# Kernel tuning notes

Hardware: AMD Instinct MI355X
Metric: run time of the kernel (lower is better)

The kernel has to match this reference:

```python
import jax, jax.numpy as jnp
import numpy as np

B, L, D_IN, H, N_BLOCKS, N_STATE, PRED = 2048, 168, 9, 96, 4, 96, 96
N2 = N_STATE // 2  # complex-conjugate pairs: keep half the state, double the real part


def s4d_kernel(log_dt, log_A_real, A_imag, C_re, C_im, length):
    # S4D (diagonal SSM) convolution kernel, ZOH-style discretization.
    dt = jnp.exp(log_dt)[:, None]                  # (H,1)
    A = -jnp.exp(log_A_real) + 1j * A_imag         # (H,N2)
    C = C_re + 1j * C_im                           # (H,N2)
    dtA = dt * A                                   # (H,N2)
    Ct = C * (jnp.exp(dtA) - 1.0) / A              # discretized C
    # Vandermonde: K[h,l] = 2*Re(sum_n Ct[h,n] * exp(dtA[h,n] * l))
    V = jnp.exp(dtA[:, :, None] * jnp.arange(length))  # (H,N2,L)
    return 2.0 * jnp.einsum('hn,hnl->hl', Ct, V).real  # (H,L)


def causal_conv(u, K):
    # u: (B,L,H), K: (H,L) -> causal depthwise convolution via FFT
    n = 2 * u.shape[1]
    Uf = jnp.fft.rfft(u, n=n, axis=1)              # (B,n/2+1,H)
    Kf = jnp.fft.rfft(K.T, n=n, axis=0)            # (n/2+1,H)
    return jnp.fft.irfft(Uf * Kf[None], n=n, axis=1)[:, :u.shape[1]]


def layer_norm(x, w, b):
    mu = x.mean(-1, keepdims=True)
    var = x.var(-1, keepdims=True)
    return (x - mu) / jnp.sqrt(var + 1e-5) * w + b


def setup_inputs() -> dict:
    key = jax.random.key(0)
    ks = jax.random.split(key, 20)
    r = lambda k, s, sc=1.0: jax.random.normal(k, s, jnp.float32) * sc
    inp = {
        'x': r(ks[0], (B, L, D_IN)),
        'enc_W': r(ks[1], (D_IN, H), 1.0 / np.sqrt(D_IN)),
        'enc_b': jnp.zeros((H,), jnp.float32),
        # per-block S4D parameters, stacked on leading n_blocks axis
        'log_dt': jax.random.uniform(ks[2], (N_BLOCKS, H), jnp.float32,
                                     np.log(1e-3), np.log(1e-1)),
        'log_A_real': jnp.full((N_BLOCKS, H, N2), np.log(0.5), jnp.float32),
        'A_imag': jnp.tile(np.pi * jnp.arange(N2, dtype=jnp.float32), (N_BLOCKS, H, 1)),
        'C_re': r(ks[3], (N_BLOCKS, H, N2), 0.5),
        'C_im': r(ks[4], (N_BLOCKS, H, N2), 0.5),
        'D_skip': r(ks[5], (N_BLOCKS, H)),
        'W_out': r(ks[6], (N_BLOCKS, H, H), 1.0 / np.sqrt(H)),
        'b_out': jnp.zeros((N_BLOCKS, H), jnp.float32),
        'ln_w': jnp.ones((N_BLOCKS, H), jnp.float32),
        'ln_b': jnp.zeros((N_BLOCKS, H), jnp.float32),
        'dec_W': r(ks[7], (H, H), 1.0 / np.sqrt(H)),
        'dec_b': jnp.zeros((H,), jnp.float32),
        'fc1_W': r(ks[8], (H * L, H), 1.0 / np.sqrt(H * L)),
        'fc1_b': jnp.zeros((H,), jnp.float32),
        'fc2_W': r(ks[9], (H, PRED), 1.0 / np.sqrt(H)),
        'fc2_b': jnp.zeros((PRED,), jnp.float32),
    }
    return inp


def reference(x, enc_W, enc_b, log_dt, log_A_real, A_imag, C_re, C_im, D_skip,
              W_out, b_out, ln_w, ln_b, dec_W, dec_b, fc1_W, fc1_b, fc2_W, fc2_b):
    h = x @ enc_W + enc_b                              # (B,L,H) encoder
    for i in range(N_BLOCKS):                          # post-norm residual S4 blocks
        K = s4d_kernel(log_dt[i], log_A_real[i], A_imag[i], C_re[i], C_im[i], L)
        z = causal_conv(h, K) + h * D_skip[i]          # SSM conv + skip D*u
        z = jax.nn.gelu(z)                             # activation (dropout off at eval)
        z = z @ W_out[i] + b_out[i]                    # output mixing
        h = layer_norm(h + z, ln_w[i], ln_b[i])        # residual + post-norm
    h = h @ dec_W + dec_b                              # S4Model decoder (d_model->d_model)
    out = h.reshape(h.shape[0], -1) @ fc1_W + fc1_b    # flatten + fc1
    out = out @ fc2_W + fc2_b                          # fc2 -> PRED_LEN
    return out[..., None]                              # (B,96,1)
```

## Files before the change

kernel.cpp:

```cpp
#include <hip/hip_runtime.h>
#include <hip/hip_bf16.h>
#include <math.h>

#define NB 4
#define B  2048
#define L  168
#define DI 9
#define H  96
#define N2 48

#define ZSTR2 132

typedef short short8 __attribute__((ext_vector_type(8)));
typedef float f32x4  __attribute__((ext_vector_type(4)));
typedef unsigned short u16x8 __attribute__((ext_vector_type(8)));
typedef unsigned short u16x4 __attribute__((ext_vector_type(4)));

__device__ __forceinline__ float gelu_f(float x) {
    float x3 = x * x * x;
    float y  = 0.7978845608028654f * (x + 0.044715f * x3);
    float ey = __expf(2.0f * y);
    float t  = 1.0f - 2.0f / (ey + 1.0f);
    return 0.5f * x * (1.0f + t);
}

__device__ __forceinline__ unsigned short bf16_rne(float x) {
    unsigned u = __float_as_uint(x);
    return (unsigned short)((u + 0x7FFFu + ((u >> 16) & 1u)) >> 16);
}
__device__ __forceinline__ float b2f(unsigned short v) {
    return __uint_as_float((unsigned)v << 16);
}

__global__ void kgen_kernel(const float* __restrict__ log_dt, const float* __restrict__ lar,
                            const float* __restrict__ aim, const float* __restrict__ cre,
                            const float* __restrict__ cim, float* __restrict__ K)
{
    const int ih   = blockIdx.x;
    const int lane = threadIdx.x;
    float ctre = 0.f, ctim = 0.f, pre = 0.f, pim = 0.f, mre = 0.f, mim = 0.f;
    if (lane < N2) {
        float dt  = expf(log_dt[ih]);
        int   idx = ih * N2 + lane;
        float reA = -expf(lar[idx]);
        float imA = aim[idx];
        float dre = dt * reA, dim = dt * imA;
        float er  = expf(dre);
        float sv, cv;
        sincosf(dim, &sv, &cv);
        mre = er * cv; mim = er * sv;
        float nre = mre - 1.0f, nim = mim;
        float den = reA * reA + imA * imA;
        float tre = (nre * reA + nim * imA) / den;
        float tim = (nim * reA - nre * imA) / den;
        float cr = cre[idx], ci = cim[idx];
        ctre = cr * tre - ci * tim;
        ctim = cr * tim + ci * tre;
        pre = 1.0f; pim = 0.0f;
    }
    float* Kr = K + ih * L;
    for (int l = 0; l < L; ++l) {
        float term = ctre * pre - ctim * pim;
        #pragma unroll
        for (int off = 32; off > 0; off >>= 1) term += __shfl_xor(term, off, 64);
        if (lane == 0) Kr[l] = 2.0f * term;
        float nr = pre * mre - pim * mim;
        float ni = pre * mim + pim * mre;
        pre = nr; pim = ni;
    }
}

__global__ void wprep_kernel(const float* __restrict__ wout, short* __restrict__ wfrag, int ntask)
{
    int idx = blockIdx.x * 256 + threadIdx.x;
    if (idx >= ntask) return;
    int layer = idx / 9216;  int rem  = idx - layer * 9216;
    int ch    = rem / 3072;  int rem2 = rem - ch * 3072;
    int m     = rem2 / 512;  int rem3 = rem2 - m * 512;
    int s     = rem3 / 256;  int rem4 = rem3 - s * 256;
    int lane  = rem4 / 4;    int d    = rem4 - lane * 4;
    int g = lane >> 4, c = lane & 15;
    int k  = ch * 32 + g * 8 + 2 * d;
    int hp = m * 16 + c;
    const float* Wl = wout + (size_t)layer * H * H;
    float w0 = Wl[k * H + hp];
    float w1 = Wl[(k + 1) * H + hp];
    unsigned short b0, b1;
    if (s == 0) { b0 = bf16_rne(w0); b1 = bf16_rne(w1); }
    else {
        unsigned short h0 = bf16_rne(w0), h1 = bf16_rne(w1);
        b0 = bf16_rne(w0 - b2f(h0));
        b1 = bf16_rne(w1 - b2f(h1));
    }
    wfrag[idx * 2]     = (short)b0;
    wfrag[idx * 2 + 1] = (short)b1;
}

__global__ void tgen_kernel(const float* __restrict__ Kg, short* __restrict__ tfrag)
{
    static const int kmaxA[11] = {0, 0, 1, 1, 2, 2, 3, 3, 4, 4, 5};
    static const int toffA[11] = {0, 1, 2, 4, 6, 9, 12, 16, 20, 25, 30};
    int idx = blockIdx.x * 256 + threadIdx.x;
    if (idx >= 96 * 66 * 64) return;
    int lane = idx & 63;
    int t    = (idx >> 6) % 66;
    int h    = (idx >> 6) / 66;
    int mi = t / 6, ki = t - mi * 6;
    if (ki > kmaxA[mi]) return;
    int g = lane >> 4, c = lane & 15;
    int row = mi * 16 + c;
    short8 a;
    #pragma unroll
    for (int j = 0; j < 8; ++j) {
        int kk = ki * 32 + g * 8 + j;
        int d  = row - kk;
        float val = (row < L && d >= 0) ? Kg[h * L + d] : 0.0f;
        a[j] = (short)bf16_rne(val);
    }
    short8* dst = (short8*)tfrag + (size_t)(h * 36 + toffA[mi] + ki) * 64;
    dst[lane] = a;
}

__launch_bounds__(256)
__global__ void wcomp_kernel(const float* __restrict__ decW, const float* __restrict__ decb,
                             const float* __restrict__ fc1W, float* __restrict__ wcs,
                             float* __restrict__ cbpart)
{
    __shared__ float Bs[96 * 100];
    const int tid = threadIdx.x;
    const int l   = blockIdx.x;
    for (int e = tid; e < 96 * 96; e += 256) {
        int h = e / 96, p = e - h * 96;
        Bs[h * 100 + p] = fc1W[(size_t)(l * 96 + h) * 96 + p];
    }
    __syncthreads();
    const int pt = tid & 31;
    const int kt = tid >> 5;
    float acc[12][3];
    #pragma unroll
    for (int kk = 0; kk < 12; ++kk)
        #pragma unroll
        for (int j = 0; j < 3; ++j) acc[kk][j] = 0.f;
    for (int h = 0; h < 96; ++h) {
        float dw[12];
        #pragma unroll
        for (int kk = 0; kk < 12; ++kk) dw[kk] = decW[(kt + 8 * kk) * 96 + h];
        float bs[3];
        #pragma unroll
        for (int j = 0; j < 3; ++j) bs[j] = Bs[h * 100 + pt + 32 * j];
        #pragma unroll
        for (int kk = 0; kk < 12; ++kk)
            #pragma unroll
            for (int j = 0; j < 3; ++j) acc[kk][j] = fmaf(dw[kk], bs[j], acc[kk][j]);
    }
    float* wl = wcs + (size_t)l * 9216;
    #pragma unroll
    for (int kk = 0; kk < 12; ++kk)
        #pragma unroll
        for (int j = 0; j < 3; ++j)
            wl[(kt + 8 * kk) * 96 + pt + 32 * j] = acc[kk][j];
    if (kt == 0) {
        #pragma unroll
        for (int j = 0; j < 3; ++j) {
            float s = 0.f;
            for (int h = 0; h < 96; ++h) s = fmaf(decb[h], Bs[h * 100 + pt + 32 * j], s);
            cbpart[l * 96 + pt + 32 * j] = s;
        }
    }
}

__global__ void cbias_red_kernel(const float* __restrict__ cbpart, const float* __restrict__ fc1b,
                                 float* __restrict__ cbias)
{
    int p = threadIdx.x;
    if (p < 96) {
        float s = fc1b[p];
        for (int l = 0; l < L; ++l) s += cbpart[l * 96 + p];
        cbias[p] = s;
    }
}

__launch_bounds__(256)
__global__ void enc2_kernel(const float* __restrict__ x, const float* __restrict__ W,
                            const float* __restrict__ bias, unsigned short* __restrict__ hb2)
{
    __shared__ float Ws[DI * H];
    __shared__ float bs[H];
    const int tid = threadIdx.x;
    const int l   = blockIdx.x;
    const int b0  = blockIdx.y * 256;
    for (int e = tid; e < DI * H; e += 256) Ws[e] = W[e];
    if (tid < H) bs[tid] = bias[tid];
    __syncthreads();
    float xv[DI];
    const float* xr = x + (size_t)(b0 + tid) * (L * DI) + l * DI;
    #pragma unroll
    for (int k = 0; k < DI; ++k) xv[k] = xr[k];
    for (int h = 0; h < H; ++h) {
        float a = bs[h];
        #pragma unroll
        for (int k = 0; k < DI; ++k) a = fmaf(xv[k], Ws[k * H + h], a);
        hb2[((size_t)h * L + l) * B + b0 + tid] = bf16_rne(a);
    }
}

__launch_bounds__(512)
__global__ void conv3_kernel(const unsigned short* __restrict__ hb2, const short* __restrict__ tfrag,
                             const float* __restrict__ Dsk, unsigned short* __restrict__ z2)
{
    static const int toffA[11] = {0, 1, 2, 4, 6, 9, 12, 16, 20, 25, 30};
    __shared__ __align__(16) unsigned short zs[192 * ZSTR2];
    const int tid  = threadIdx.x;
    const int w    = tid >> 6;
    const int lane = tid & 63;
    const int g    = lane >> 4;
    const int cc   = lane & 15;
    const int h    = blockIdx.x;
    const int b0   = blockIdx.y * 128;

    for (int e = tid; e < 168 * 16; e += 512) {
        int lp = e >> 4, b8 = e & 15;
        u16x8 v = *(const u16x8*)(hb2 + ((size_t)h * L + lp) * B + b0 + b8 * 8);
        *(u16x4*)(&zs[lp * ZSTR2 + b8 * 8])     = (u16x4){v[0], v[1], v[2], v[3]};
        *(u16x4*)(&zs[lp * ZSTR2 + b8 * 8 + 4]) = (u16x4){v[4], v[5], v[6], v[7]};
    }
    for (int e = tid; e < 24 * 16; e += 512) {
        int lp = 168 + (e >> 4), b8 = e & 15;
        *(u16x4*)(&zs[lp * ZSTR2 + b8 * 8])     = (u16x4){0, 0, 0, 0};
        *(u16x4*)(&zs[lp * ZSTR2 + b8 * 8 + 4]) = (u16x4){0, 0, 0, 0};
    }
    __syncthreads();

    f32x4 acc[11];
    #pragma unroll
    for (int mi = 0; mi < 11; ++mi) acc[mi] = (f32x4){0.f, 0.f, 0.f, 0.f};

    const int col = w * 16 + cc;

    #pragma unroll
    for (int ki = 0; ki < 6; ++ki) {
        short8 bh;
        #pragma unroll
        for (int j = 0; j < 8; ++j)
            bh[j] = (short)zs[(ki * 32 + g * 8 + j) * ZSTR2 + col];
        #pragma unroll
        for (int mi = 2 * ki; mi < 11; ++mi) {
            const short8* Tf = (const short8*)(tfrag) + (size_t)(h * 36 + toffA[mi] + ki) * 64;
            short8 ah = Tf[lane];
            acc[mi] = __builtin_amdgcn_mfma_f32_16x16x32_bf16(ah, bh, acc[mi], 0, 0, 0);
        }
    }

    const float ds = Dsk[h];
    #pragma unroll
    for (int mi = 0; mi < 11; ++mi) {
        #pragma unroll
        for (int r = 0; r < 4; ++r) {
            int l = mi * 16 + g * 4 + r;
            if (l < L) {
                float uu = b2f(zs[l * ZSTR2 + col]);
                float zv = gelu_f(fmaf(ds, uu, acc[mi][r]));
                zs[l * ZSTR2 + col] = bf16_rne(zv);
            }
        }
    }
    __syncthreads();
    for (int e = tid; e < 168 * 16; e += 512) {
        int lp = e >> 4, b8 = e & 15;
        u16x4 a = *(const u16x4*)(&zs[lp * ZSTR2 + b8 * 8]);
        u16x4 b = *(const u16x4*)(&zs[lp * ZSTR2 + b8 * 8 + 4]);
        u16x8 v = {a[0], a[1], a[2], a[3], b[0], b[1], b[2], b[3]};
        *(u16x8*)(z2 + ((size_t)h * L + lp) * B + b0 + b8 * 8) = v;
    }
}

__launch_bounds__(512)
__global__ void mix2_kernel(const unsigned short* __restrict__ z2, unsigned short* __restrict__ hb2,
                            const short* __restrict__ wfrag, const float* __restrict__ bout,
                            const float* __restrict__ lnw, const float* __restrict__ lnb)
{
    __shared__ __align__(16) unsigned short zs[H * ZSTR2];
    __shared__ __align__(16) unsigned short rs[H * ZSTR2];
    const int tid  = threadIdx.x;
    const int w    = tid >> 6;
    const int lane = tid & 63;
    const int g    = lane >> 4;
    const int cc   = lane & 15;
    const int l    = blockIdx.x;
    const int b0   = blockIdx.y * 128;

    for (int e = tid; e < 96 * 16; e += 512) {
        int hh = e >> 4, b8 = e & 15;
        u16x8 v = *(const u16x8*)(z2 + ((size_t)hh * L + l) * B + b0 + b8 * 8);
        *(u16x4*)(&zs[hh * ZSTR2 + b8 * 8])     = (u16x4){v[0], v[1], v[2], v[3]};
        *(u16x4*)(&zs[hh * ZSTR2 + b8 * 8 + 4]) = (u16x4){v[4], v[5], v[6], v[7]};
    }
    for (int e = tid; e < 96 * 16; e += 512) {
        int hh = e >> 4, b8 = e & 15;
        u16x8 v = *(const u16x8*)(hb2 + ((size_t)hh * L + l) * B + b0 + b8 * 8);
        *(u16x4*)(&rs[hh * ZSTR2 + b8 * 8])     = (u16x4){v[0], v[1], v[2], v[3]};
        *(u16x4*)(&rs[hh * ZSTR2 + b8 * 8 + 4]) = (u16x4){v[4], v[5], v[6], v[7]};
    }
    __syncthreads();

    f32x4 acc[6];
    #pragma unroll
    for (int m = 0; m < 6; ++m) acc[m] = (f32x4){0.f, 0.f, 0.f, 0.f};

    const int col = w * 16 + cc;

    #pragma unroll
    for (int ks = 0; ks < 3; ++ks) {
        short8 bh;
        #pragma unroll
        for (int j = 0; j < 8; ++j)
            bh[j] = (short)zs[(ks * 32 + g * 8 + j) * ZSTR2 + col];
        const short8* Wf = (const short8*)(wfrag) + ks * 12 * 64;
        #pragma unroll
        for (int m = 0; m < 6; ++m) {
            short8 ah = Wf[(m * 2 + 0) * 64 + lane];
            short8 al = Wf[(m * 2 + 1) * 64 + lane];
            acc[m] = __builtin_amdgcn_mfma_f32_16x16x32_bf16(al, bh, acc[m], 0, 0, 0);
            acc[m] = __builtin_amdgcn_mfma_f32_16x16x32_bf16(ah, bh, acc[m], 0, 0, 0);
        }
    }

    float vals[6][4];
    float s = 0.f, q = 0.f;
    #pragma unroll
    for (int m = 0; m < 6; ++m) {
        float4 B4 = *(const float4*)(bout + m * 16 + g * 4);
        float bo[4] = {B4.x, B4.y, B4.z, B4.w};
        #pragma unroll
        for (int r = 0; r < 4; ++r) {
            int hr = m * 16 + g * 4 + r;
            float res = b2f(rs[hr * ZSTR2 + col]);
            float v = acc[m][r] + bo[r] + res;
            vals[m][r] = v;
            s += v; q += v * v;
        }
    }
    s += __shfl_xor(s, 16, 64); q += __shfl_xor(q, 16, 64);
    s += __shfl_xor(s, 32, 64); q += __shfl_xor(q, 32, 64);
    float mean = s * (1.0f / 96.0f);
    float var  = q * (1.0f / 96.0f) - mean * mean;
    float rstd = rsqrtf(var + 1e-5f);
    #pragma unroll
    for (int m = 0; m < 6; ++m) {
        float4 W4 = *(const float4*)(lnw + m * 16 + g * 4);
        float4 Bb = *(const float4*)(lnb + m * 16 + g * 4);
        float wv[4] = {W4.x, W4.y, W4.z, W4.w};
        float bv[4] = {Bb.x, Bb.y, Bb.z, Bb.w};
        #pragma unroll
        for (int r = 0; r < 4; ++r) {
            int hr = m * 16 + g * 4 + r;
            rs[hr * ZSTR2 + col] = bf16_rne(fmaf((vals[m][r] - mean) * rstd, wv[r], bv[r]));
        }
    }
    __syncthreads();
    for (int e = tid; e < 96 * 16; e += 512) {
        int hh = e >> 4, b8 = e & 15;
        u16x4 a = *(const u16x4*)(&rs[hh * ZSTR2 + b8 * 8]);
        u16x4 b = *(const u16x4*)(&rs[hh * ZSTR2 + b8 * 8 + 4]);
        u16x8 v = {a[0], a[1], a[2], a[3], b[0], b[1], b[2], b[3]};
        *(u16x8*)(hb2 + ((size_t)hh * L + l) * B + b0 + b8 * 8) = v;
    }
}

__launch_bounds__(256)
__global__ void fc1m_kernel(const unsigned short* __restrict__ hb2, const short* __restrict__ wcfrag,
                            float* __restrict__ partial)
{
    __shared__ __align__(16) unsigned short zs[H * ZSTR2];
    const int tid  = threadIdx.x;
    const int w    = tid >> 6;
    const int lane = tid & 63;
    const int g    = lane >> 4;
    const int cc   = lane & 15;
    const int ksp  = blockIdx.x;
    const int b0   = blockIdx.y * 128;

    f32x4 acc[2][6];
    #pragma unroll
    for (int n2 = 0; n2 < 2; ++n2)
        #pragma unroll
        for (int m = 0; m < 6; ++m) acc[n2][m] = (f32x4){0.f, 0.f, 0.f, 0.f};

    for (int il = 0; il < 4; ++il) {
        const int l = ksp * 4 + il;
        __syncthreads();
        for (int e = tid; e < 96 * 16; e += 256) {
            int hh = e >> 4, b8 = e & 15;
            u16x8 v = *(const u16x8*)(hb2 + ((size_t)hh * L + l) * B + b0 + b8 * 8);
            *(u16x4*)(&zs[hh * ZSTR2 + b8 * 8])     = (u16x4){v[0], v[1], v[2], v[3]};
            *(u16x4*)(&zs[hh * ZSTR2 + b8 * 8 + 4]) = (u16x4){v[4], v[5], v[6], v[7]};
        }
        __syncthreads();
        for (int ksl = 0; ksl < 3; ++ksl) {
            short8 bh[2];
            #pragma unroll
            for (int n2 = 0; n2 < 2; ++n2) {
                int col = (w * 2 + n2) * 16 + cc;
                #pragma unroll
                for (int j = 0; j < 8; ++j)
                    bh[n2][j] = (short)zs[(ksl * 32 + g * 8 + j) * ZSTR2 + col];
            }
            const short8* Wf = (const short8*)(wcfrag) + (size_t)(l * 3 + ksl) * 768;
            #pragma unroll
            for (int m = 0; m < 6; ++m) {
                short8 ah = Wf[(m * 2 + 0) * 64 + lane];
                short8 al = Wf[(m * 2 + 1) * 64 + lane];
                #pragma unroll
                for (int n2 = 0; n2 < 2; ++n2) {
                    acc[n2][m] = __builtin_amdgcn_mfma_f32_16x16x32_bf16(al, bh[n2], acc[n2][m], 0, 0, 0);
                    acc[n2][m] = __builtin_amdgcn_mfma_f32_16x16x32_bf16(ah, bh[n2], acc[n2][m], 0, 0, 0);
                }
            }
        }
    }

    #pragma unroll
    for (int n2 = 0; n2 < 2; ++n2) {
        int gb = b0 + (w * 2 + n2) * 16 + cc;
        #pragma unroll
        for (int m = 0; m < 6; ++m) {
            *(float4*)&partial[((size_t)ksp * B + gb) * 96 + m * 16 + g * 4] =
                make_float4(acc[n2][m][0], acc[n2][m][1], acc[n2][m][2], acc[n2][m][3]);
        }
    }
}

__global__ void fc1red_kernel(const float* __restrict__ partial, const float* __restrict__ cbias,
                              float* __restrict__ t1)
{
    int o = blockIdx.x * 256 + threadIdx.x;
    int p = o % 96;
    float s = cbias[p];
    #pragma unroll 6
    for (int k = 0; k < 42; ++k) s += partial[(size_t)k * (B * 96) + o];
    t1[o] = s;
}

__launch_bounds__(256)
__global__ void fc2_kernel(const float* __restrict__ t1, const float* __restrict__ W,
                           const float* __restrict__ fb, float* __restrict__ out)
{
    __shared__ float Ws[96 * 100];
    const int tid = threadIdx.x;
    for (int e = tid; e < 96 * 96; e += 256) Ws[(e / 96) * 100 + (e % 96)] = W[e];
    __syncthreads();
    int o = blockIdx.x * 256 + tid;
    int b = o / 96, p = o - b * 96;
    const float* tr = t1 + b * 96;
    float acc = fb[p];
    #pragma unroll 4
    for (int h = 0; h < 96; ++h) acc = fmaf(tr[h], Ws[h * 100 + p], acc);
    out[o] = acc;
}

extern "C" void kernel_launch(void* const* d_in, const int* in_sizes, int n_in,
                              void* d_out, int out_size, void* d_ws, size_t ws_size,
                              hipStream_t stream)
{
    const float* x      = (const float*)d_in[0];
    const float* encW   = (const float*)d_in[1];
    const float* encb   = (const float*)d_in[2];
    const float* log_dt = (const float*)d_in[3];
    const float* lar    = (const float*)d_in[4];
    const float* aim    = (const float*)d_in[5];
    const float* cre    = (const float*)d_in[6];
    const float* cim    = (const float*)d_in[7];
    const float* dsk    = (const float*)d_in[8];
    const float* wout   = (const float*)d_in[9];
    const float* boutp  = (const float*)d_in[10];
    const float* lnw    = (const float*)d_in[11];
    const float* lnb    = (const float*)d_in[12];
    const float* decW   = (const float*)d_in[13];
    const float* decb   = (const float*)d_in[14];
    const float* fc1W   = (const float*)d_in[15];
    const float* fc1b   = (const float*)d_in[16];
    const float* fc2W   = (const float*)d_in[17];
    const float* fc2b   = (const float*)d_in[18];

    char*           ws      = (char*)d_ws;
    float*          K       = (float*)(ws);
    short*          wfrag   = (short*)(ws + ((size_t)384 << 10));
    float*          t1      = (float*)(ws + ((size_t)1 << 20));
    float*          cbpart  = (float*)(ws + ((size_t)1 << 20) + (900 << 10));
    float*          cbias   = (float*)(ws + ((size_t)1 << 20) + (980 << 10));
    short*          wcfrag  = (short*)(ws + ((size_t)2 << 20));
    short*          tfrag   = (short*)(ws + ((size_t)9 << 20));
    float*          wcs     = (float*)(ws + ((size_t)9 << 20));
    unsigned short* hb2     = (unsigned short*)(ws + ((size_t)16 << 20));
    unsigned short* z2      = (unsigned short*)(ws + ((size_t)80 << 20));
    float*          partial = (float*)(ws + ((size_t)80 << 20));

    kgen_kernel<<<NB * H, 64, 0, stream>>>(log_dt, lar, aim, cre, cim, K);
    wprep_kernel<<<144, 256, 0, stream>>>(wout, wfrag, NB * 9216);
    wcomp_kernel<<<L, 256, 0, stream>>>(decW, decb, fc1W, wcs, cbpart);
    wprep_kernel<<<6048, 256, 0, stream>>>(wcs, wcfrag, L * 9216);
    cbias_red_kernel<<<1, 128, 0, stream>>>(cbpart, fc1b, cbias);
    enc2_kernel<<<dim3(L, 8), 256, 0, stream>>>(x, encW, encb, hb2);
    for (int i = 0; i < NB; ++i) {
        tgen_kernel<<<1584, 256, 0, stream>>>(K + i * H * L, tfrag);
        conv3_kernel<<<dim3(H, 16), 512, 0, stream>>>(hb2, tfrag, dsk + i * H, z2);
        mix2_kernel<<<dim3(L, 16), 512, 0, stream>>>(z2, hb2, wfrag + i * 18432,
                                                     boutp + i * H, lnw + i * H, lnb + i * H);
    }
    fc1m_kernel<<<dim3(42, 16), 256, 0, stream>>>(hb2, wcfrag, partial);
    fc1red_kernel<<<768, 256, 0, stream>>>(partial, cbias, t1);
    fc2_kernel<<<768, 256, 0, stream>>>(t1, fc2W, fc2b, (float*)d_out);
}
```

Baseline: 569.6 us.

## Shrink conv tiles, batch weight-fragment loads, and simplify GELU evaluation

The conv kernel now uses 256-thread blocks covering 64 batch columns instead of 128, with a smaller LDS tile, launching twice as many blocks and hinting four blocks per SM, which should raise occupancy. In the conv, mix and fc1 kernels, all weight fragments for an MFMA step are loaded into registers before the MFMA chain, so memory latency overlaps with compute instead of interleaving load and MFMA. GELU is rewritten as x*sigmoid using hardware exp2 and rcp intrinsics, cutting instruction count for slightly different rounding. The batched loads raise register pressure, and the smaller conv tiles reread the per-h T fragments more often.

```diff
diff --git a/kernel.cpp b/kernel.cpp
--- a/kernel.cpp
+++ b/kernel.cpp
@@ -10,6 +10,7 @@
 #define N2 48
 
 #define ZSTR2 132
+#define CZ 68
 
 typedef short short8 __attribute__((ext_vector_type(8)));
 typedef float f32x4  __attribute__((ext_vector_type(4)));
@@ -17,11 +18,10 @@
 typedef unsigned short u16x4 __attribute__((ext_vector_type(4)));
 
 __device__ __forceinline__ float gelu_f(float x) {
-    float x3 = x * x * x;
-    float y  = 0.7978845608028654f * (x + 0.044715f * x3);
-    float ey = __expf(2.0f * y);
-    float t  = 1.0f - 2.0f / (ey + 1.0f);
-    return 0.5f * x * (1.0f + t);
+    float x2 = x * x;
+    float e  = __builtin_amdgcn_exp2f(x * fmaf(0.1029432225f, x2, 2.3022081899f));
+    float r  = __builtin_amdgcn_rcpf(e + 1.0f);
+    return x * (1.0f - r);
 }
 
 __device__ __forceinline__ unsigned short bf16_rne(float x) {
@@ -204,30 +204,30 @@
     }
 }
 
-__launch_bounds__(512)
+__launch_bounds__(256, 4)
 __global__ void conv3_kernel(const unsigned short* __restrict__ hb2, const short* __restrict__ tfrag,
                              const float* __restrict__ Dsk, unsigned short* __restrict__ z2)
 {
     static const int toffA[11] = {0, 1, 2, 4, 6, 9, 12, 16, 20, 25, 30};
-    __shared__ __align__(16) unsigned short zs[192 * ZSTR2];
+    __shared__ __align__(16) unsigned short zs[192 * CZ];
     const int tid  = threadIdx.x;
     const int w    = tid >> 6;
     const int lane = tid & 63;
     const int g    = lane >> 4;
     const int cc   = lane & 15;
     const int h    = blockIdx.x;
-    const int b0   = blockIdx.y * 128;
-
-    for (int e = tid; e < 168 * 16; e += 512) {
-        int lp = e >> 4, b8 = e & 15;
+    const int b0   = blockIdx.y * 64;
+
+    for (int e = tid; e < 168 * 8; e += 256) {
+        int lp = e >> 3, b8 = e & 7;
         u16x8 v = *(const u16x8*)(hb2 + ((size_t)h * L + lp) * B + b0 + b8 * 8);
-        *(u16x4*)(&zs[lp * ZSTR2 + b8 * 8])     = (u16x4){v[0], v[1], v[2], v[3]};
-        *(u16x4*)(&zs[lp * ZSTR2 + b8 * 8 + 4]) = (u16x4){v[4], v[5], v[6], v[7]};
-    }
-    for (int e = tid; e < 24 * 16; e += 512) {
-        int lp = 168 + (e >> 4), b8 = e & 15;
-        *(u16x4*)(&zs[lp * ZSTR2 + b8 * 8])     = (u16x4){0, 0, 0, 0};
-        *(u16x4*)(&zs[lp * ZSTR2 + b8 * 8 + 4]) = (u16x4){0, 0, 0, 0};
+        *(u16x4*)(&zs[lp * CZ + b8 * 8])     = (u16x4){v[0], v[1], v[2], v[3]};
+        *(u16x4*)(&zs[lp * CZ + b8 * 8 + 4]) = (u16x4){v[4], v[5], v[6], v[7]};
+    }
+    for (int e = tid; e < 24 * 8; e += 256) {
+        int lp = 168 + (e >> 3), b8 = e & 7;
+        *(u16x4*)(&zs[lp * CZ + b8 * 8])     = (u16x4){0, 0, 0, 0};
+        *(u16x4*)(&zs[lp * CZ + b8 * 8 + 4]) = (u16x4){0, 0, 0, 0};
     }
     __syncthreads();
 
@@ -236,19 +236,23 @@
     for (int mi = 0; mi < 11; ++mi) acc[mi] = (f32x4){0.f, 0.f, 0.f, 0.f};
 
     const int col = w * 16 + cc;
+    const short8* Tbase = (const short8*)tfrag + (size_t)h * 36 * 64 + lane;
 
     #pragma unroll
     for (int ki = 0; ki < 6; ++ki) {
         short8 bh;
         #pragma unroll
         for (int j = 0; j < 8; ++j)
-            bh[j] = (short)zs[(ki * 32 + g * 8 + j) * ZSTR2 + col];
-        #pragma unroll
-        for (int mi = 2 * ki; mi < 11; ++mi) {
-            const short8* Tf = (const short8*)(tfrag) + (size_t)(h * 36 + toffA[mi] + ki) * 64;
-            short8 ah = Tf[lane];
-            acc[mi] = __builtin_amdgcn_mfma_f32_16x16x32_bf16(ah, bh, acc[mi], 0, 0, 0);
-        }
+            bh[j] = (short)zs[(ki * 32 + g * 8 + j) * CZ + col];
+        short8 tf[11];
+        #pragma unroll
+        for (int mi = 0; mi < 11; ++mi)
+            if (mi >= 2 * ki)
+                tf[mi] = Tbase[(size_t)(toffA[mi] + ki) * 64];
+        #pragma unroll
+        for (int mi = 0; mi < 11; ++mi)
+            if (mi >= 2 * ki)
+                acc[mi] = __builtin_amdgcn_mfma_f32_16x16x32_bf16(tf[mi], bh, acc[mi], 0, 0, 0);
     }
 
     const float ds = Dsk[h];
@@ -258,17 +262,17 @@
         for (int r = 0; r < 4; ++r) {
             int l = mi * 16 + g * 4 + r;
             if (l < L) {
-                float uu = b2f(zs[l * ZSTR2 + col]);
+                float uu = b2f(zs[l * CZ + col]);
                 float zv = gelu_f(fmaf(ds, uu, acc[mi][r]));
-                zs[l * ZSTR2 + col] = bf16_rne(zv);
+                zs[l * CZ + col] = bf16_rne(zv);
             }
         }
     }
     __syncthreads();
-    for (int e = tid; e < 168 * 16; e += 512) {
-        int lp = e >> 4, b8 = e & 15;
-        u16x4 a = *(const u16x4*)(&zs[lp * ZSTR2 + b8 * 8]);
-        u16x4 b = *(const u16x4*)(&zs[lp * ZSTR2 + b8 * 8 + 4]);
+    for (int e = tid; e < 168 * 8; e += 256) {
+        int lp = e >> 3, b8 = e & 7;
+        u16x4 a = *(const u16x4*)(&zs[lp * CZ + b8 * 8]);
+        u16x4 b = *(const u16x4*)(&zs[lp * CZ + b8 * 8 + 4]);
         u16x8 v = {a[0], a[1], a[2], a[3], b[0], b[1], b[2], b[3]};
         *(u16x8*)(z2 + ((size_t)h * L + lp) * B + b0 + b8 * 8) = v;
     }
@@ -316,12 +320,13 @@
         for (int j = 0; j < 8; ++j)
             bh[j] = (short)zs[(ks * 32 + g * 8 + j) * ZSTR2 + col];
         const short8* Wf = (const short8*)(wfrag) + ks * 12 * 64;
+        short8 wa[12];
+        #pragma unroll
+        for (int m = 0; m < 12; ++m) wa[m] = Wf[m * 64 + lane];
         #pragma unroll
         for (int m = 0; m < 6; ++m) {
-            short8 ah = Wf[(m * 2 + 0) * 64 + lane];
-            short8 al = Wf[(m * 2 + 1) * 64 + lane];
-            acc[m] = __builtin_amdgcn_mfma_f32_16x16x32_bf16(al, bh, acc[m], 0, 0, 0);
-            acc[m] = __builtin_amdgcn_mfma_f32_16x16x32_bf16(ah, bh, acc[m], 0, 0, 0);
+            acc[m] = __builtin_amdgcn_mfma_f32_16x16x32_bf16(wa[2 * m + 1], bh, acc[m], 0, 0, 0);
+            acc[m] = __builtin_amdgcn_mfma_f32_16x16x32_bf16(wa[2 * m],     bh, acc[m], 0, 0, 0);
         }
     }
 
@@ -406,14 +411,15 @@
                     bh[n2][j] = (short)zs[(ksl * 32 + g * 8 + j) * ZSTR2 + col];
             }
             const short8* Wf = (const short8*)(wcfrag) + (size_t)(l * 3 + ksl) * 768;
+            short8 wa[12];
+            #pragma unroll
+            for (int m = 0; m < 12; ++m) wa[m] = Wf[m * 64 + lane];
             #pragma unroll
             for (int m = 0; m < 6; ++m) {
-                short8 ah = Wf[(m * 2 + 0) * 64 + lane];
-                short8 al = Wf[(m * 2 + 1) * 64 + lane];
                 #pragma unroll
                 for (int n2 = 0; n2 < 2; ++n2) {
-                    acc[n2][m] = __builtin_amdgcn_mfma_f32_16x16x32_bf16(al, bh[n2], acc[n2][m], 0, 0, 0);
-                    acc[n2][m] = __builtin_amdgcn_mfma_f32_16x16x32_bf16(ah, bh[n2], acc[n2][m], 0, 0, 0);
+                    acc[n2][m] = __builtin_amdgcn_mfma_f32_16x16x32_bf16(wa[2 * m + 1], bh[n2], acc[n2][m], 0, 0, 0);
+                    acc[n2][m] = __builtin_amdgcn_mfma_f32_16x16x32_bf16(wa[2 * m],     bh[n2], acc[n2][m], 0, 0, 0);
                 }
             }
         }
@@ -503,7 +509,7 @@
     enc2_kernel<<<dim3(L, 8), 256, 0, stream>>>(x, encW, encb, hb2);
     for (int i = 0; i < NB; ++i) {
         tgen_kernel<<<1584, 256, 0, stream>>>(K + i * H * L, tfrag);
-        conv3_kernel<<<dim3(H, 16), 512, 0, stream>>>(hb2, tfrag, dsk + i * H, z2);
+        conv3_kernel<<<dim3(H, 32), 256, 0, stream>>>(hb2, tfrag, dsk + i * H, z2);
         mix2_kernel<<<dim3(L, 16), 512, 0, stream>>>(z2, hb2, wfrag + i * 18432,
                                                      boutp + i * H, lnw + i * H, lnb + i * H);
     }
```

After: 526.6 us. -7.6%, faster.
